# Performance work log

Hardware: AMD Instinct MI355X
Metric: run time of the kernel (lower is better)

Reference implementation:

```python
import jax, jax.numpy as jnp
import numpy as np

B, T, I, H, L = 32768, 30, 4, 64, 32


def _lstm_layer(x, Wih, Whh, bih, bhh):
    """PyTorch-semantics single-layer LSTM, batch_first. Returns (outputs [B,T,H], h_T [B,H])."""
    # Precompute input contribution for all timesteps: [B, T, 4H]
    xg = jnp.einsum('bti,gi->btg', x, Wih) + bih + bhh
    Hh = Whh.shape[1]
    h0 = jnp.zeros((x.shape[0], Hh), x.dtype)

    def step(carry, xg_t):
        h, c = carry
        g = xg_t + h @ Whh.T  # [B, 4H]
        i, f, gg, o = jnp.split(g, 4, axis=-1)  # PyTorch gate order i,f,g,o
        c = jax.nn.sigmoid(f) * c + jax.nn.sigmoid(i) * jnp.tanh(gg)
        h = jax.nn.sigmoid(o) * jnp.tanh(c)
        return (h, c), h

    (hT, _), hs = jax.lax.scan(step, (h0, h0), jnp.swapaxes(xg, 0, 1))
    return jnp.swapaxes(hs, 0, 1), hT


def setup_inputs() -> dict:
    key = jax.random.key(0)
    ks = jax.random.split(key, 20)
    s = 0.1  # weight scale for numerical stability
    inp = {
        'x': jax.random.normal(ks[0], (B, T, I), jnp.float32),
        'enc1_Wih': s * jax.random.normal(ks[1], (4 * H, I), jnp.float32),
        'enc1_Whh': s * jax.random.normal(ks[2], (4 * H, H), jnp.float32),
        'enc1_bih': s * jax.random.normal(ks[3], (4 * H,), jnp.float32),
        'enc1_bhh': s * jax.random.normal(ks[4], (4 * H,), jnp.float32),
        'enc2_Wih': s * jax.random.normal(ks[5], (4 * L, H), jnp.float32),
        'enc2_Whh': s * jax.random.normal(ks[6], (4 * L, L), jnp.float32),
        'enc2_bih': s * jax.random.normal(ks[7], (4 * L,), jnp.float32),
        'enc2_bhh': s * jax.random.normal(ks[8], (4 * L,), jnp.float32),
        'dec1_Wih': s * jax.random.normal(ks[9], (4 * H, L), jnp.float32),
        'dec1_Whh': s * jax.random.normal(ks[10], (4 * H, H), jnp.float32),
        'dec1_bih': s * jax.random.normal(ks[11], (4 * H,), jnp.float32),
        'dec1_bhh': s * jax.random.normal(ks[12], (4 * H,), jnp.float32),
        'dec2_Wih': s * jax.random.normal(ks[13], (4 * I, H), jnp.float32),
        'dec2_Whh': s * jax.random.normal(ks[14], (4 * I, I), jnp.float32),
        'dec2_bih': s * jax.random.normal(ks[15], (4 * I,), jnp.float32),
        'dec2_bhh': s * jax.random.normal(ks[16], (4 * I,), jnp.float32),
    }
    return inp


def reference(x, enc1_Wih, enc1_Whh, enc1_bih, enc1_bhh,
              enc2_Wih, enc2_Whh, enc2_bih, enc2_bhh,
              dec1_Wih, dec1_Whh, dec1_bih, dec1_bhh,
              dec2_Wih, dec2_Whh, dec2_bih, dec2_bhh):
    seq_len = x.shape[1]
    out, _ = _lstm_layer(x, enc1_Wih, enc1_Whh, enc1_bih, enc1_bhh)
    out, h = _lstm_layer(out, enc2_Wih, enc2_Whh, enc2_bih, enc2_bhh)
    latent = jnp.repeat(h[:, None, :], seq_len, axis=1)  # [B, T, L]
    out, _ = _lstm_layer(latent, dec1_Wih, dec1_Whh, dec1_bih, dec1_bhh)
    out, _ = _lstm_layer(out, dec2_Wih, dec2_Whh, dec2_bih, dec2_bhh)
    return out
```

## Files before the change

kernel.cpp:

```cpp
#include <hip/hip_runtime.h>
#include <stdint.h>


typedef unsigned short u16;
typedef unsigned int u32;
typedef __attribute__((ext_vector_type(8))) short bf16x8;
typedef __attribute__((ext_vector_type(4))) short s16x4;
typedef __attribute__((ext_vector_type(4))) float f32x4;

#define BATCH 32768
#define TT 30
#define IN 4
#define WAVES 16
#define BLOCKT (WAVES * 64)
#define MB 16
#define NPAIR 8
#define BPB (NPAIR * MB)

#define LOG2E 1.4426950408889634f
#define LOG2E2 2.8853900817779268f

#define WREG 18432
#define O_WHH1HI 0
#define O_W1FOLD 8192
#define O_WIH2HI 12288
#define O_WHH2HI 16384
#define O_WHH3HI 0
#define O_WIH3HI 8192
#define O_WIH4HI 12288
#define O_W4HHF  12800

#define NBIAS 400
#define PBUF 1600
#define SMEM_WORDS (WREG + NBIAS + NPAIR * PBUF)
#define SMEM_BYTES (SMEM_WORDS * 4)

#define WB() __builtin_amdgcn_wave_barrier()
#define MFMA(a, b, c) __builtin_amdgcn_mfma_f32_16x16x32_bf16((a), (b), (c), 0, 0, 0)

__device__ __forceinline__ u16 f2bf(float f) {
    u32 u = __float_as_uint(f);
    u += 0x7fffu + ((u >> 16) & 1u);
    return (u16)(u >> 16);
}
__device__ __forceinline__ float bf2f(u16 v) { return __uint_as_float(((u32)v) << 16); }
__device__ __forceinline__ float sigY(float y) {
    return __builtin_amdgcn_rcpf(1.f + __builtin_amdgcn_exp2f(-y));
}
__device__ __forceinline__ float tanhY(float y) {
    return fmaf(-2.f, __builtin_amdgcn_rcpf(__builtin_amdgcn_exp2f(y) + 1.f), 1.f);
}
__device__ __forceinline__ float tanhC(float c) { return tanhY(c * LOG2E2); }

template <int KT, int GS>
__device__ __forceinline__ void stageBh(u16* hi, const float* src, int N, int tid) {
    const int K = KT * 32;
    const int total = N * K;
    for (int idx = tid; idx < total; idx += BLOCKT) {
        const int j = idx & 7;
        const int l = (idx >> 3) & 63;
        const int pr = idx >> 9;
        const int kt = pr & (KT - 1);
        const int nt = pr / KT;
        const int n = (nt << 4) | (l & 15);
        const int k = (kt << 5) + ((l >> 4) << 3) + j;
        const float s = (((n >> GS) & 3) == 2) ? LOG2E2 : LOG2E;
        hi[idx] = f2bf(src[n * K + k] * s);
    }
}

__device__ __forceinline__ f32x4 splat4(float b) {
    f32x4 v = {b, b, b, b};
    return v;
}

__global__ __launch_bounds__(BLOCKT)
__attribute__((amdgpu_waves_per_eu(4, 4)))
void lstm_ae(
    const float* __restrict__ x,
    const float* __restrict__ w1ih, const float* __restrict__ w1hh,
    const float* __restrict__ b1i, const float* __restrict__ b1h,
    const float* __restrict__ w2ih, const float* __restrict__ w2hh,
    const float* __restrict__ b2i, const float* __restrict__ b2h,
    const float* __restrict__ w3ih, const float* __restrict__ w3hh,
    const float* __restrict__ b3i, const float* __restrict__ b3h,
    const float* __restrict__ w4ih, const float* __restrict__ w4hh,
    const float* __restrict__ b4i, const float* __restrict__ b4h,
    float* __restrict__ out) {
    extern __shared__ float smem[];
    float* W = smem;
    float* biasF = smem + WREG;
    float* bufs = biasF + NBIAS;

    const int tid = threadIdx.x;
    const int wave = tid >> 6, lane = tid & 63;
    const int pair = wave & 7, role = wave >> 3;
    const int col = lane & 15, quad = lane >> 4;

    float* pb = bufs + pair * PBUF;
    u16* h1d = (u16*)pb;
    u16* h2b = (u16*)(pb + 1024);
    u16* xfold = (u16*)(pb + 1280);
    float* gbuf = pb + 1280;
    float* bufH4 = pb + 1536;

    const int b0w = blockIdx.x * BPB + pair * MB;

    stageBh<2, 6>((u16*)(W + O_WHH1HI), w1hh, 256, tid);
    stageBh<2, 5>((u16*)(W + O_WIH2HI), w2ih, 128, tid);
    stageBh<1, 5>((u16*)(W + O_WHH2HI), w2hh, 128, tid);
    {
        u16* F = (u16*)(W + O_W1FOLD);
        for (int idx = tid; idx < 16 * 512; idx += BLOCKT) {
            const int nt = idx >> 9;
            const int rem = idx & 511;
            const int l = rem >> 3;
            const int j = rem & 7;
            const int q = l >> 4;
            const int n = (nt << 4) | (l & 15);
            const float s = ((n >> 6) == 2) ? LOG2E2 : LOG2E;
            u16 v = 0;
            if (q == 0) {
                v = f2bf(w1ih[n * 4 + (j & 3)] * s);
            } else if (q == 1) {
                if (j < 4) {
                    const float w = w1ih[n * 4 + j] * s;
                    v = f2bf(w - bf2f(f2bf(w)));
                } else if (j == 4) {
                    v = f2bf((b1i[n] + b1h[n]) * s);
                } else if (j == 5) {
                    const float b = (b1i[n] + b1h[n]) * s;
                    v = f2bf(b - bf2f(f2bf(b)));
                }
            }
            F[idx] = v;
        }
    }
    for (int i = tid; i < 128; i += BLOCKT)
        biasF[i] = (b2i[i] + b2h[i]) * ((((i >> 5) & 3) == 2) ? LOG2E2 : LOG2E);
    for (int i = tid; i < 256; i += BLOCKT)
        biasF[128 + i] = (b3i[i] + b3h[i]) * ((((i >> 6) & 3) == 2) ? LOG2E2 : LOG2E);
    for (int i = tid; i < 16; i += BLOCKT)
        biasF[384 + i] = (b4i[i] + b4h[i]) * ((((i >> 2) & 3) == 2) ? LOG2E2 : LOG2E);
    {
        u32* z = (u32*)pb;
        if (role == 0) {
            for (int i = lane; i < 1024; i += 64) z[i] = 0u;
            for (int i = lane; i < 256; i += 64) z[1280 + i] = 0u;
        } else {
            for (int i = lane; i < 256; i += 64) z[1024 + i] = 0u;
            if (lane < 64) bufH4[lane] = 0.f;
        }
    }
    WB();
    if (role == 0 && quad == 1) {
        xfold[lane * 8 + 4] = (u16)0x3F80;
        xfold[lane * 8 + 5] = (u16)0x3F80;
    }
    __syncthreads();

    const u16* Whh1hi = (const u16*)(W + O_WHH1HI);
    const u16* W1fold = (const u16*)(W + O_W1FOLD);
    const u16* Wih2hi = (const u16*)(W + O_WIH2HI);
    const u16* Whh2hi = (const u16*)(W + O_WHH2HI);

    float c1[4][4];
    float c2[2][4];
#pragma unroll
    for (int q = 0; q < 4; ++q)
#pragma unroll
        for (int r = 0; r < 4; ++r) c1[q][r] = 0.f;
#pragma unroll
    for (int q = 0; q < 2; ++q)
#pragma unroll
        for (int r = 0; r < 4; ++r) c2[q][r] = 0.f;

    const f32x4 zf = {0.f, 0.f, 0.f, 0.f};
    float4 xcur;
    if (role == 0)
        xcur = *reinterpret_cast<const float4*>(x + ((size_t)(b0w + col) * TT + 0) * IN);

    for (int s = 0; s <= TT; ++s) {
        if (role == 0) {
            if (s < TT) {
                {
                    const u16 xh0 = f2bf(xcur.x), xh1 = f2bf(xcur.y);
                    const u16 xh2 = f2bf(xcur.z), xh3 = f2bf(xcur.w);
                    if (quad == 0) {
                        bf16x8 v;
                        v[0] = (short)xh0; v[1] = (short)xh1; v[2] = (short)xh2; v[3] = (short)xh3;
                        v[4] = (short)f2bf(xcur.x - bf2f(xh0));
                        v[5] = (short)f2bf(xcur.y - bf2f(xh1));
                        v[6] = (short)f2bf(xcur.z - bf2f(xh2));
                        v[7] = (short)f2bf(xcur.w - bf2f(xh3));
                        *reinterpret_cast<bf16x8*>(xfold + lane * 8) = v;
                    } else if (quad == 1) {
                        s16x4 v;
                        v[0] = (short)xh0; v[1] = (short)xh1; v[2] = (short)xh2; v[3] = (short)xh3;
                        *reinterpret_cast<s16x4*>(xfold + lane * 8) = v;
                    }
                }
                WB();
                {
                    const int tn = (s + 1 < TT) ? s + 1 : s;
                    xcur = *reinterpret_cast<const float4*>(
                        x + ((size_t)(b0w + col) * TT + tn) * IN);
                }
                const u16* hprev = h1d + (((s + 1) & 1) << 10);
                u16* hout = h1d + ((s & 1) << 10);
                const bf16x8 a1h0 = *reinterpret_cast<const bf16x8*>(hprev + lane * 8);
                const bf16x8 a1h1 = *reinterpret_cast<const bf16x8*>(hprev + (64 + lane) * 8);
                const bf16x8 a1x = *reinterpret_cast<const bf16x8*>(xfold + lane * 8);
#pragma unroll
                for (int q = 0; q < 4; ++q) {
                    f32x4 acc[4];
#pragma unroll
                    for (int i = 0; i < 4; ++i) {
                        const int nt = i * 4 + q;
                        const bf16x8 bx = *reinterpret_cast<const bf16x8*>(W1fold + (nt * 64 + lane) * 8);
                        const bf16x8 bh0 = *reinterpret_cast<const bf16x8*>(Whh1hi + ((nt * 2 + 0) * 64 + lane) * 8);
                        const bf16x8 bh1 = *reinterpret_cast<const bf16x8*>(Whh1hi + ((nt * 2 + 1) * 64 + lane) * 8);
                        f32x4 a = MFMA(a1x, bx, zf);
                        a = MFMA(a1h0, bh0, a);
                        a = MFMA(a1h1, bh1, a);
                        acc[i] = a;
                    }
                    const int kt = q >> 1;
                    const int lup = ((((q & 1) << 1) + (col >> 3)) << 4);
                    const int j = col & 7;
#pragma unroll
                    for (int r = 0; r < 4; ++r) {
                        const int m = quad * 4 + r;
                        const float iv = sigY(acc[0][r]);
                        const float fv = sigY(acc[1][r]);
                        const float gv = tanhY(acc[2][r]);
                        const float ov = sigY(acc[3][r]);
                        c1[q][r] = fv * c1[q][r] + iv * gv;
                        const float h = ov * tanhC(c1[q][r]);
                        hout[(kt * 64 + m + lup) * 8 + j] = f2bf(h);
                    }
                }
            }
        } else {
            if (s >= 1) {
                const u16* hprev = h1d + (((s + 1) & 1) << 10);
                const bf16x8 a1h0 = *reinterpret_cast<const bf16x8*>(hprev + lane * 8);
                const bf16x8 a1h1 = *reinterpret_cast<const bf16x8*>(hprev + (64 + lane) * 8);
                const bf16x8 a2h = *reinterpret_cast<const bf16x8*>(h2b + lane * 8);
                f32x4 acc2[8];
#pragma unroll
                for (int nt = 0; nt < 8; ++nt) {
                    const bf16x8 bh0 = *reinterpret_cast<const bf16x8*>(Wih2hi + ((nt * 2 + 0) * 64 + lane) * 8);
                    const bf16x8 bh1 = *reinterpret_cast<const bf16x8*>(Wih2hi + ((nt * 2 + 1) * 64 + lane) * 8);
                    const bf16x8 ch = *reinterpret_cast<const bf16x8*>(Whh2hi + (nt * 64 + lane) * 8);
                    f32x4 a = splat4(biasF[nt * 16 + col]);
                    a = MFMA(a1h0, bh0, a);
                    a = MFMA(a1h1, bh1, a);
                    a = MFMA(a2h, ch, a);
                    acc2[nt] = a;
                }
                WB();
#pragma unroll
                for (int q = 0; q < 2; ++q) {
                    const int lup = (((q << 1) + (col >> 3)) << 4);
                    const int j = col & 7;
#pragma unroll
                    for (int r = 0; r < 4; ++r) {
                        const int m = quad * 4 + r;
                        const float iv = sigY(acc2[q][r]);
                        const float fv = sigY(acc2[2 + q][r]);
                        const float gv = tanhY(acc2[4 + q][r]);
                        const float ov = sigY(acc2[6 + q][r]);
                        c2[q][r] = fv * c2[q][r] + iv * gv;
                        const float h = ov * tanhC(c2[q][r]);
                        h2b[(m + lup) * 8 + j] = f2bf(h);
                    }
                }
            }
        }
        __syncthreads();
    }

    stageBh<2, 6>((u16*)(W + O_WHH3HI), w3hh, 256, tid);
    stageBh<1, 6>((u16*)(W + O_WIH3HI), w3ih, 256, tid);
    stageBh<2, 2>((u16*)(W + O_WIH4HI), w4ih, 16, tid);
    for (int i = tid; i < 64; i += BLOCKT)
        W[O_W4HHF + i] = w4hh[i] * ((((i >> 4) & 3) == 2) ? LOG2E2 : LOG2E);
    if (role == 0) {
        u32* z = (u32*)pb;
        for (int i = lane; i < 1024; i += 64) z[i] = 0u;
    } else {
        if (lane < 64) bufH4[lane] = 0.f;
    }
    __syncthreads();

    const u16* Whh3hi = (const u16*)(W + O_WHH3HI);
    const u16* Wih3hi = (const u16*)(W + O_WIH3HI);
    const u16* Wih4hi = (const u16*)(W + O_WIH4HI);
    const float* W4hhF = W + O_W4HHF;

    float c3[4][4];
    float c4 = 0.f, bias4r = 0.f;
    bf16x8 aLh;
    if (role == 0) {
#pragma unroll
        for (int q = 0; q < 4; ++q)
#pragma unroll
            for (int r = 0; r < 4; ++r) c3[q][r] = 0.f;
        aLh = *reinterpret_cast<const bf16x8*>(h2b + lane * 8);
    } else {
        bias4r = biasF[384 + col];
    }
    const int u4 = lane & 3, mb = lane >> 2;

    for (int s = 0; s <= TT; ++s) {
        if (role == 0) {
            if (s < TT) {
                const u16* hprev = h1d + (((s + 1) & 1) << 10);
                u16* hout = h1d + ((s & 1) << 10);
                const bf16x8 a3h0 = *reinterpret_cast<const bf16x8*>(hprev + lane * 8);
                const bf16x8 a3h1 = *reinterpret_cast<const bf16x8*>(hprev + (64 + lane) * 8);
#pragma unroll
                for (int q = 0; q < 4; ++q) {
                    f32x4 acc[4];
#pragma unroll
                    for (int i = 0; i < 4; ++i) {
                        const int nt = i * 4 + q;
                        const bf16x8 bL = *reinterpret_cast<const bf16x8*>(Wih3hi + (nt * 64 + lane) * 8);
                        const bf16x8 bh0 = *reinterpret_cast<const bf16x8*>(Whh3hi + ((nt * 2 + 0) * 64 + lane) * 8);
                        const bf16x8 bh1 = *reinterpret_cast<const bf16x8*>(Whh3hi + ((nt * 2 + 1) * 64 + lane) * 8);
                        f32x4 a = MFMA(aLh, bL, splat4(biasF[128 + nt * 16 + col]));
                        a = MFMA(a3h0, bh0, a);
                        a = MFMA(a3h1, bh1, a);
                        acc[i] = a;
                    }
                    const int kt = q >> 1;
                    const int lup = ((((q & 1) << 1) + (col >> 3)) << 4);
                    const int j = col & 7;
#pragma unroll
                    for (int r = 0; r < 4; ++r) {
                        const int m = quad * 4 + r;
                        const float iv = sigY(acc[0][r]);
                        const float fv = sigY(acc[1][r]);
                        const float gv = tanhY(acc[2][r]);
                        const float ov = sigY(acc[3][r]);
                        c3[q][r] = fv * c3[q][r] + iv * gv;
                        const float h = ov * tanhC(c3[q][r]);
                        hout[(kt * 64 + m + lup) * 8 + j] = f2bf(h);
                    }
                }
            }
        } else {
            if (s >= 1) {
                const int t = s - 1;
                const u16* hprev = h1d + (((s + 1) & 1) << 10);
                const bf16x8 a3h0 = *reinterpret_cast<const bf16x8*>(hprev + lane * 8);
                const bf16x8 a3h1 = *reinterpret_cast<const bf16x8*>(hprev + (64 + lane) * 8);
                f32x4 acc4 = splat4(bias4r);
                {
                    const float4 w4 = *reinterpret_cast<const float4*>(W4hhF + col * 4);
#pragma unroll
                    for (int r = 0; r < 4; ++r) {
                        const float4 hv = *reinterpret_cast<const float4*>(bufH4 + (quad * 4 + r) * 4);
                        float sa = acc4[r];
                        sa = fmaf(w4.x, hv.x, sa);
                        sa = fmaf(w4.y, hv.y, sa);
                        sa = fmaf(w4.z, hv.z, sa);
                        sa = fmaf(w4.w, hv.w, sa);
                        acc4[r] = sa;
                    }
                }
                {
                    const bf16x8 bh0 = *reinterpret_cast<const bf16x8*>(Wih4hi + (0 * 64 + lane) * 8);
                    const bf16x8 bh1 = *reinterpret_cast<const bf16x8*>(Wih4hi + (1 * 64 + lane) * 8);
                    acc4 = MFMA(a3h0, bh0, acc4);
                    acc4 = MFMA(a3h1, bh1, acc4);
                }
                WB();
#pragma unroll
                for (int r = 0; r < 4; ++r) gbuf[(quad * 4 + r) * 16 + col] = acc4[r];
                WB();
                {
                    const float iv = sigY(gbuf[mb * 16 + u4]);
                    const float fv = sigY(gbuf[mb * 16 + 4 + u4]);
                    const float gv = tanhY(gbuf[mb * 16 + 8 + u4]);
                    const float ov = sigY(gbuf[mb * 16 + 12 + u4]);
                    c4 = fv * c4 + iv * gv;
                    const float h = ov * tanhC(c4);
                    out[((size_t)(b0w + mb) * TT + t) * IN + u4] = h;
                    bufH4[mb * 4 + u4] = h;
                }
                WB();
            }
        }
        __syncthreads();
    }
}

extern "C" void kernel_launch(void* const* d_in, const int* in_sizes, int n_in,
                              void* d_out, int out_size, void* d_ws, size_t ws_size,
                              hipStream_t stream) {
    (void)in_sizes; (void)n_in; (void)d_ws; (void)ws_size; (void)out_size;
    hipFuncSetAttribute(reinterpret_cast<const void*>(lstm_ae),
                        hipFuncAttributeMaxDynamicSharedMemorySize, SMEM_BYTES);
    const float* xi = (const float*)d_in[0];
    const float* w1ih = (const float*)d_in[1];
    const float* w1hh = (const float*)d_in[2];
    const float* b1i = (const float*)d_in[3];
    const float* b1h = (const float*)d_in[4];
    const float* w2ih = (const float*)d_in[5];
    const float* w2hh = (const float*)d_in[6];
    const float* b2i = (const float*)d_in[7];
    const float* b2h = (const float*)d_in[8];
    const float* w3ih = (const float*)d_in[9];
    const float* w3hh = (const float*)d_in[10];
    const float* b3i = (const float*)d_in[11];
    const float* b3h = (const float*)d_in[12];
    const float* w4ih = (const float*)d_in[13];
    const float* w4hh = (const float*)d_in[14];
    const float* b4i = (const float*)d_in[15];
    const float* b4h = (const float*)d_in[16];
    float* out = (float*)d_out;

    lstm_ae<<<dim3(BATCH / BPB), dim3(BLOCKT), SMEM_BYTES, stream>>>(
        xi, w1ih, w1hh, b1i, b1h, w2ih, w2hh, b2i, b2h,
        w3ih, w3hh, b3i, b3h, w4ih, w4hh, b4i, b4h, out);
}
```

Measured before the change: 315.9 us.

## Transpose MFMA operands, fuse LSTM gate math with shared reciprocal, pack bf16 stores

Swaps the A/B operands of every MFMA so each lane holds four consecutive hidden units of one batch row. That enables packed 8-byte bf16 stores of h via v_cvt_pk_bf16_f32 and vector bias loads. Gate nonlinearities are algebraically merged so each cell update uses five exp2 and two reciprocals instead of five separate rcp calls. The x split into hi/lo bf16 parts is now built in registers rather than staged through LDS, which also drops a wave barrier. The merged formulas risk overflow or precision loss when exponentials are large.

Measured after the change: 289.1 us. -8.5%, faster.

```diff
diff --git a/kernel.cpp b/kernel.cpp
--- a/kernel.cpp
+++ b/kernel.cpp
@@ -5,8 +5,9 @@
 typedef unsigned short u16;
 typedef unsigned int u32;
 typedef __attribute__((ext_vector_type(8))) short bf16x8;
-typedef __attribute__((ext_vector_type(4))) short s16x4;
 typedef __attribute__((ext_vector_type(4))) float f32x4;
+typedef __attribute__((ext_vector_type(4))) u32 u32x4;
+typedef __attribute__((ext_vector_type(2))) u32 u32x2;
 
 #define BATCH 32768
 #define TT 30
@@ -44,13 +45,25 @@
     return (u16)(u >> 16);
 }
 __device__ __forceinline__ float bf2f(u16 v) { return __uint_as_float(((u32)v) << 16); }
-__device__ __forceinline__ float sigY(float y) {
-    return __builtin_amdgcn_rcpf(1.f + __builtin_amdgcn_exp2f(-y));
-}
-__device__ __forceinline__ float tanhY(float y) {
-    return fmaf(-2.f, __builtin_amdgcn_rcpf(__builtin_amdgcn_exp2f(y) + 1.f), 1.f);
-}
-__device__ __forceinline__ float tanhC(float c) { return tanhY(c * LOG2E2); }
+
+__device__ __forceinline__ u32 cvtpk2(float a, float b) {
+    u32 d;
+    asm("v_cvt_pk_bf16_f32 %0, %1, %2" : "=v"(d) : "v"(a), "v"(b));
+    return d;
+}
+
+__device__ __forceinline__ float unitH(float yi, float yf, float yg, float yo, float& c) {
+    const float ei = __builtin_amdgcn_exp2f(-yi);
+    const float ef = __builtin_amdgcn_exp2f(-yf);
+    const float eg = __builtin_amdgcn_exp2f(yg);
+    const float eo = __builtin_amdgcn_exp2f(-yo);
+    const float Z = (1.f + ei) * (1.f + eg);
+    const float X = 1.f + ef;
+    const float num = fmaf(eg - 1.f, X, c * Z);
+    c = num * __builtin_amdgcn_rcpf(X * Z);
+    const float ec = __builtin_amdgcn_exp2f(c * LOG2E2);
+    return (ec - 1.f) * __builtin_amdgcn_rcpf((1.f + eo) * (1.f + ec));
+}
 
 template <int KT, int GS>
 __device__ __forceinline__ void stageBh(u16* hi, const float* src, int N, int tid) {
@@ -67,11 +80,6 @@
         const float s = (((n >> GS) & 3) == 2) ? LOG2E2 : LOG2E;
         hi[idx] = f2bf(src[n * K + k] * s);
     }
-}
-
-__device__ __forceinline__ f32x4 splat4(float b) {
-    f32x4 v = {b, b, b, b};
-    return v;
 }
 
 __global__ __launch_bounds__(BLOCKT)
@@ -100,11 +108,11 @@
     float* pb = bufs + pair * PBUF;
     u16* h1d = (u16*)pb;
     u16* h2b = (u16*)(pb + 1024);
-    u16* xfold = (u16*)(pb + 1280);
     float* gbuf = pb + 1280;
     float* bufH4 = pb + 1536;
 
     const int b0w = blockIdx.x * BPB + pair * MB;
+    const int hbase = (col << 3) + ((quad & 1) << 2) + ((quad >> 1) << 7);
 
     stageBh<2, 6>((u16*)(W + O_WHH1HI), w1hh, 256, tid);
     stageBh<2, 5>((u16*)(W + O_WIH2HI), w2ih, 128, tid);
@@ -146,16 +154,10 @@
         u32* z = (u32*)pb;
         if (role == 0) {
             for (int i = lane; i < 1024; i += 64) z[i] = 0u;
-            for (int i = lane; i < 256; i += 64) z[1280 + i] = 0u;
         } else {
             for (int i = lane; i < 256; i += 64) z[1024 + i] = 0u;
-            if (lane < 64) bufH4[lane] = 0.f;
+            bufH4[lane] = 0.f;
         }
-    }
-    WB();
-    if (role == 0 && quad == 1) {
-        xfold[lane * 8 + 4] = (u16)0x3F80;
-        xfold[lane * 8 + 5] = (u16)0x3F80;
     }
     __syncthreads();
 
@@ -183,24 +185,20 @@
     for (int s = 0; s <= TT; ++s) {
         if (role == 0) {
             if (s < TT) {
-                {
-                    const u16 xh0 = f2bf(xcur.x), xh1 = f2bf(xcur.y);
-                    const u16 xh2 = f2bf(xcur.z), xh3 = f2bf(xcur.w);
-                    if (quad == 0) {
-                        bf16x8 v;
-                        v[0] = (short)xh0; v[1] = (short)xh1; v[2] = (short)xh2; v[3] = (short)xh3;
-                        v[4] = (short)f2bf(xcur.x - bf2f(xh0));
-                        v[5] = (short)f2bf(xcur.y - bf2f(xh1));
-                        v[6] = (short)f2bf(xcur.z - bf2f(xh2));
-                        v[7] = (short)f2bf(xcur.w - bf2f(xh3));
-                        *reinterpret_cast<bf16x8*>(xfold + lane * 8) = v;
-                    } else if (quad == 1) {
-                        s16x4 v;
-                        v[0] = (short)xh0; v[1] = (short)xh1; v[2] = (short)xh2; v[3] = (short)xh3;
-                        *reinterpret_cast<s16x4*>(xfold + lane * 8) = v;
-                    }
-                }
-                WB();
+                const u32 hi01 = cvtpk2(xcur.x, xcur.y);
+                const u32 hi23 = cvtpk2(xcur.z, xcur.w);
+                const float r0 = xcur.x - __uint_as_float(hi01 << 16);
+                const float r1 = xcur.y - __uint_as_float(hi01 & 0xffff0000u);
+                const float r2 = xcur.z - __uint_as_float(hi23 << 16);
+                const float r3 = xcur.w - __uint_as_float(hi23 & 0xffff0000u);
+                const u32 lo01 = cvtpk2(r0, r1);
+                const u32 lo23 = cvtpk2(r2, r3);
+                u32x4 xv;
+                xv.x = (quad <= 1) ? hi01 : 0u;
+                xv.y = (quad <= 1) ? hi23 : 0u;
+                xv.z = (quad == 0) ? lo01 : ((quad == 1) ? 0x3F803F80u : 0u);
+                xv.w = (quad == 0) ? lo23 : 0u;
+                const bf16x8 a1x = __builtin_bit_cast(bf16x8, xv);
                 {
                     const int tn = (s + 1 < TT) ? s + 1 : s;
                     xcur = *reinterpret_cast<const float4*>(
@@ -210,7 +208,6 @@
                 u16* hout = h1d + ((s & 1) << 10);
                 const bf16x8 a1h0 = *reinterpret_cast<const bf16x8*>(hprev + lane * 8);
                 const bf16x8 a1h1 = *reinterpret_cast<const bf16x8*>(hprev + (64 + lane) * 8);
-                const bf16x8 a1x = *reinterpret_cast<const bf16x8*>(xfold + lane * 8);
 #pragma unroll
                 for (int q = 0; q < 4; ++q) {
                     f32x4 acc[4];
@@ -220,25 +217,19 @@
                         const bf16x8 bx = *reinterpret_cast<const bf16x8*>(W1fold + (nt * 64 + lane) * 8);
                         const bf16x8 bh0 = *reinterpret_cast<const bf16x8*>(Whh1hi + ((nt * 2 + 0) * 64 + lane) * 8);
                         const bf16x8 bh1 = *reinterpret_cast<const bf16x8*>(Whh1hi + ((nt * 2 + 1) * 64 + lane) * 8);
-                        f32x4 a = MFMA(a1x, bx, zf);
-                        a = MFMA(a1h0, bh0, a);
-                        a = MFMA(a1h1, bh1, a);
+                        f32x4 a = MFMA(bx, a1x, zf);
+                        a = MFMA(bh0, a1h0, a);
+                        a = MFMA(bh1, a1h1, a);
                         acc[i] = a;
                     }
-                    const int kt = q >> 1;
-                    const int lup = ((((q & 1) << 1) + (col >> 3)) << 4);
-                    const int j = col & 7;
-#pragma unroll
-                    for (int r = 0; r < 4; ++r) {
-                        const int m = quad * 4 + r;
-                        const float iv = sigY(acc[0][r]);
-                        const float fv = sigY(acc[1][r]);
-                        const float gv = tanhY(acc[2][r]);
-                        const float ov = sigY(acc[3][r]);
-                        c1[q][r] = fv * c1[q][r] + iv * gv;
-                        const float h = ov * tanhC(c1[q][r]);
-                        hout[(kt * 64 + m + lup) * 8 + j] = f2bf(h);
-                    }
+                    const float h0 = unitH(acc[0][0], acc[1][0], acc[2][0], acc[3][0], c1[q][0]);
+                    const float h1 = unitH(acc[0][1], acc[1][1], acc[2][1], acc[3][1], c1[q][1]);
+                    const float h2 = unitH(acc[0][2], acc[1][2], acc[2][2], acc[3][2], c1[q][2]);
+                    const float h3 = unitH(acc[0][3], acc[1][3], acc[2][3], acc[3][3], c1[q][3]);
+                    u32x2 wv;
+                    wv.x = cvtpk2(h0, h1);
+                    wv.y = cvtpk2(h2, h3);
+                    *reinterpret_cast<u32x2*>(hout + hbase + ((q >> 1) << 9) + ((q & 1) << 8)) = wv;
                 }
             }
         } else {
@@ -253,28 +244,23 @@
                     const bf16x8 bh0 = *reinterpret_cast<const bf16x8*>(Wih2hi + ((nt * 2 + 0) * 64 + lane) * 8);
                     const bf16x8 bh1 = *reinterpret_cast<const bf16x8*>(Wih2hi + ((nt * 2 + 1) * 64 + lane) * 8);
                     const bf16x8 ch = *reinterpret_cast<const bf16x8*>(Whh2hi + (nt * 64 + lane) * 8);
-                    f32x4 a = splat4(biasF[nt * 16 + col]);
-                    a = MFMA(a1h0, bh0, a);
-                    a = MFMA(a1h1, bh1, a);
-                    a = MFMA(a2h, ch, a);
+                    f32x4 a = *reinterpret_cast<const f32x4*>(biasF + nt * 16 + (quad << 2));
+                    a = MFMA(bh0, a1h0, a);
+                    a = MFMA(bh1, a1h1, a);
+                    a = MFMA(ch, a2h, a);
                     acc2[nt] = a;
                 }
                 WB();
 #pragma unroll
                 for (int q = 0; q < 2; ++q) {
-                    const int lup = (((q << 1) + (col >> 3)) << 4);
-                    const int j = col & 7;
-#pragma unroll
-                    for (int r = 0; r < 4; ++r) {
-                        const int m = quad * 4 + r;
-                        const float iv = sigY(acc2[q][r]);
-                        const float fv = sigY(acc2[2 + q][r]);
-                        const float gv = tanhY(acc2[4 + q][r]);
-                        const float ov = sigY(acc2[6 + q][r]);
-                        c2[q][r] = fv * c2[q][r] + iv * gv;
-                        const float h = ov * tanhC(c2[q][r]);
-                        h2b[(m + lup) * 8 + j] = f2bf(h);
-                    }
+                    const float h0 = unitH(acc2[q][0], acc2[2 + q][0], acc2[4 + q][0], acc2[6 + q][0], c2[q][0]);
+                    const float h1 = unitH(acc2[q][1], acc2[2 + q][1], acc2[4 + q][1], acc2[6 + q][1], c2[q][1]);
+                    const float h2 = unitH(acc2[q][2], acc2[2 + q][2], acc2[4 + q][2], acc2[6 + q][2], c2[q][2]);
+                    const float h3 = unitH(acc2[q][3], acc2[2 + q][3], acc2[4 + q][3], acc2[6 + q][3], c2[q][3]);
+                    u32x2 wv;
+                    wv.x = cvtpk2(h0, h1);
+                    wv.y = cvtpk2(h2, h3);
+                    *reinterpret_cast<u32x2*>(h2b + hbase + (q << 8)) = wv;
                 }
             }
         }
@@ -290,7 +276,7 @@
         u32* z = (u32*)pb;
         for (int i = lane; i < 1024; i += 64) z[i] = 0u;
     } else {
-        if (lane < 64) bufH4[lane] = 0.f;
+        bufH4[lane] = 0.f;
     }
     __syncthreads();
 
@@ -300,7 +286,8 @@
     const float* W4hhF = W + O_W4HHF;
 
     float c3[4][4];
-    float c4 = 0.f, bias4r = 0.f;
+    float c4 = 0.f;
+    f32x4 bias4v = zf;
     bf16x8 aLh;
     if (role == 0) {
 #pragma unroll
@@ -309,7 +296,7 @@
             for (int r = 0; r < 4; ++r) c3[q][r] = 0.f;
         aLh = *reinterpret_cast<const bf16x8*>(h2b + lane * 8);
     } else {
-        bias4r = biasF[384 + col];
+        bias4v = *reinterpret_cast<const f32x4*>(biasF + 384 + (quad << 2));
     }
     const int u4 = lane & 3, mb = lane >> 2;
 
@@ -329,25 +316,20 @@
                         const bf16x8 bL = *reinterpret_cast<const bf16x8*>(Wih3hi + (nt * 64 + lane) * 8);
                         const bf16x8 bh0 = *reinterpret_cast<const bf16x8*>(Whh3hi + ((nt * 2 + 0) * 64 + lane) * 8);
                         const bf16x8 bh1 = *reinterpret_cast<const bf16x8*>(Whh3hi + ((nt * 2 + 1) * 64 + lane) * 8);
-                        f32x4 a = MFMA(aLh, bL, splat4(biasF[128 + nt * 16 + col]));
-                        a = MFMA(a3h0, bh0, a);
-                        a = MFMA(a3h1, bh1, a);
+                        f32x4 a = *reinterpret_cast<const f32x4*>(biasF + 128 + nt * 16 + (quad << 2));
+                        a = MFMA(bL, aLh, a);
+                        a = MFMA(bh0, a3h0, a);
+                        a = MFMA(bh1, a3h1, a);
                         acc[i] = a;
                     }
-                    const int kt = q >> 1;
-                    const int lup = ((((q & 1) << 1) + (col >> 3)) << 4);
-                    const int j = col & 7;
-#pragma unroll
-                    for (int r = 0; r < 4; ++r) {
-                        const int m = quad * 4 + r;
-                        const float iv = sigY(acc[0][r]);
-                        const float fv = sigY(acc[1][r]);
-                        const float gv = tanhY(acc[2][r]);
-                        const float ov = sigY(acc[3][r]);
-                        c3[q][r] = fv * c3[q][r] + iv * gv;
-                        const float h = ov * tanhC(c3[q][r]);
-                        hout[(kt * 64 + m + lup) * 8 + j] = f2bf(h);
-                    }
+                    const float h0 = unitH(acc[0][0], acc[1][0], acc[2][0], acc[3][0], c3[q][0]);
+                    const float h1 = unitH(acc[0][1], acc[1][1], acc[2][1], acc[3][1], c3[q][1]);
+                    const float h2 = unitH(acc[0][2], acc[1][2], acc[2][2], acc[3][2], c3[q][2]);
+                    const float h3 = unitH(acc[0][3], acc[1][3], acc[2][3], acc[3][3], c3[q][3]);
+                    u32x2 wv;
+                    wv.x = cvtpk2(h0, h1);
+                    wv.y = cvtpk2(h2, h3);
+                    *reinterpret_cast<u32x2*>(hout + hbase + ((q >> 1) << 9) + ((q & 1) << 8)) = wv;
                 }
             }
         } else {
@@ -356,12 +338,12 @@
                 const u16* hprev = h1d + (((s + 1) & 1) << 10);
                 const bf16x8 a3h0 = *reinterpret_cast<const bf16x8*>(hprev + lane * 8);
                 const bf16x8 a3h1 = *reinterpret_cast<const bf16x8*>(hprev + (64 + lane) * 8);
-                f32x4 acc4 = splat4(bias4r);
+                f32x4 acc4 = bias4v;
                 {
-                    const float4 w4 = *reinterpret_cast<const float4*>(W4hhF + col * 4);
+                    const float4 hv = *reinterpret_cast<const float4*>(bufH4 + (col << 2));
 #pragma unroll
                     for (int r = 0; r < 4; ++r) {
-                        const float4 hv = *reinterpret_cast<const float4*>(bufH4 + (quad * 4 + r) * 4);
+                        const float4 w4 = *reinterpret_cast<const float4*>(W4hhF + ((quad * 4 + r) << 2));
                         float sa = acc4[r];
                         sa = fmaf(w4.x, hv.x, sa);
                         sa = fmaf(w4.y, hv.y, sa);
@@ -373,20 +355,18 @@
                 {
                     const bf16x8 bh0 = *reinterpret_cast<const bf16x8*>(Wih4hi + (0 * 64 + lane) * 8);
                     const bf16x8 bh1 = *reinterpret_cast<const bf16x8*>(Wih4hi + (1 * 64 + lane) * 8);
-                    acc4 = MFMA(a3h0, bh0, acc4);
-                    acc4 = MFMA(a3h1, bh1, acc4);
+                    acc4 = MFMA(bh0, a3h0, acc4);
+                    acc4 = MFMA(bh1, a3h1, acc4);
                 }
                 WB();
-#pragma unroll
-                for (int r = 0; r < 4; ++r) gbuf[(quad * 4 + r) * 16 + col] = acc4[r];
+                *reinterpret_cast<f32x4*>(gbuf + (col << 4) + (quad << 2)) = acc4;
                 WB();
                 {
-                    const float iv = sigY(gbuf[mb * 16 + u4]);
-                    const float fv = sigY(gbuf[mb * 16 + 4 + u4]);
-                    const float gv = tanhY(gbuf[mb * 16 + 8 + u4]);
-                    const float ov = sigY(gbuf[mb * 16 + 12 + u4]);
-                    c4 = fv * c4 + iv * gv;
-                    const float h = ov * tanhC(c4);
+                    const float yi = gbuf[mb * 16 + u4];
+                    const float yf = gbuf[mb * 16 + 4 + u4];
+                    const float yg = gbuf[mb * 16 + 8 + u4];
+                    const float yo = gbuf[mb * 16 + 12 + u4];
+                    const float h = unitH(yi, yf, yg, yo, c4);
                     out[((size_t)(b0w + mb) * TT + t) * IN + u4] = h;
                     bufH4[mb * 4 + u4] = h;
                 }
```
